# Kernel optimization log

Measured on AMD Instinct MI355X. Metric: run time of the kernel, lower is better.

## Reference

```python
import jax, jax.numpy as jnp
import numpy as np

N_USERS = 50000
N_ENTITIES = 100000
CHANNEL = 64
N_FACTORS = 4
N_REL = 9  # n_relations; weight has N_REL-1 rows
N_EDGES = 1_500_000
NNZ = 800_000
N_HOPS = 2


def _l2_normalize(x, eps=1e-12):
    # matches torch F.normalize(dim=1)
    n = jnp.sqrt(jnp.sum(x * x, axis=1, keepdims=True))
    return x / jnp.maximum(n, eps)


def _distance_correlation(t1, t2):
    # t1, t2: [d] rows of disen_weight_att (d = n_relations-1)
    ch = t1.shape[0]
    t1 = t1[:, None]
    t2 = t2[:, None]
    a_ = (t1 @ t1.T) * 2.0
    b_ = (t2 @ t2.T) * 2.0
    t1s = t1 ** 2
    t2s = t2 ** 2
    a = jnp.sqrt(jnp.maximum(t1s - a_ + t1s.T, 0.0) + 1e-8)
    b = jnp.sqrt(jnp.maximum(t2s - b_ + t2s.T, 0.0) + 1e-8)
    A = a - a.mean(axis=0, keepdims=True) - a.mean(axis=1, keepdims=True) + a.mean()
    B = b - b.mean(axis=0, keepdims=True) - b.mean(axis=1, keepdims=True) + b.mean()
    dcov_AB = jnp.sqrt(jnp.maximum((A * B).sum() / ch ** 2, 0.0) + 1e-8)
    dcov_AA = jnp.sqrt(jnp.maximum((A * A).sum() / ch ** 2, 0.0) + 1e-8)
    dcov_BB = jnp.sqrt(jnp.maximum((B * B).sum() / ch ** 2, 0.0) + 1e-8)
    return dcov_AB / jnp.sqrt(dcov_AA * dcov_BB + 1e-8)


def _cul_cor(disen_weight_att):
    cor = jnp.asarray(0.0, disen_weight_att.dtype)
    for i in range(N_FACTORS):
        for j in range(i + 1, N_FACTORS):
            cor = cor + _distance_correlation(disen_weight_att[i], disen_weight_att[j])
    return cor


def setup_inputs() -> dict:
    key = jax.random.key(0)
    ks = jax.random.split(key, 11)
    return {
        "user_emb": jax.random.normal(ks[0], (N_USERS, CHANNEL), jnp.float32) * 0.1,
        "entity_emb": jax.random.normal(ks[1], (N_ENTITIES, CHANNEL), jnp.float32) * 0.1,
        "latent_emb": jax.random.normal(ks[2], (N_FACTORS, CHANNEL), jnp.float32) * 0.1,
        "weight": jax.random.normal(ks[3], (N_REL - 1, CHANNEL), jnp.float32) * 0.1,
        "disen_weight_att": jax.random.normal(ks[4], (N_FACTORS, N_REL - 1), jnp.float32) * 0.1,
        "interact_vals": jax.random.uniform(ks[5], (NNZ,), jnp.float32),
        "head": jax.random.randint(ks[6], (N_EDGES,), 0, N_ENTITIES),
        "tail": jax.random.randint(ks[7], (N_EDGES,), 0, N_ENTITIES),
        "edge_type": jax.random.randint(ks[8], (N_EDGES,), 1, N_REL),  # in [1, N_REL-1]
        "interact_rows": jax.random.randint(ks[9], (NNZ,), 0, N_USERS),
        "interact_cols": jax.random.randint(ks[10], (NNZ,), 0, N_ENTITIES),
    }


def reference(user_emb, entity_emb, latent_emb, weight, disen_weight_att,
              interact_vals, head, tail, edge_type, interact_rows, interact_cols):
    n_entities = entity_emb.shape[0]
    n_users = user_emb.shape[0]
    cor = _cul_cor(disen_weight_att)

    entity_res = entity_emb
    user_res = user_emb
    ones_e = jnp.ones((head.shape[0],), entity_emb.dtype)
    cnt = jax.ops.segment_sum(ones_e, head, num_segments=n_entities)  # reused: head fixed
    cnt = jnp.maximum(cnt, 1.0)[:, None]

    for _ in range(N_HOPS):
        # KG aggregate: gather tail emb * relation emb, scatter-mean by head
        rel_emb = weight[edge_type - 1]                      # [E, C]
        msg = entity_emb[tail] * rel_emb                     # [E, C]
        entity_agg = jax.ops.segment_sum(msg, head, num_segments=n_entities) / cnt

        # user -> latent factor attention
        score = jax.nn.softmax(user_emb @ latent_emb.T, axis=1)   # [U, F]

        # user aggregate: sparse.mm(interact_mat, entity_emb)
        gathered = interact_vals[:, None] * entity_emb[interact_cols]  # [nnz, C]
        user_agg = jax.ops.segment_sum(gathered, interact_rows, num_segments=n_users)

        disen_weight = jax.nn.softmax(disen_weight_att, axis=-1) @ weight  # [F, C]
        mix = score @ disen_weight                                          # [U, C]
        user_new = user_agg * mix + user_agg

        entity_emb = _l2_normalize(entity_agg)
        user_emb = _l2_normalize(user_new)
        entity_res = entity_res + entity_emb
        user_res = user_res + user_emb

    return entity_res, user_res, cor
```

## Files before the change

kernel.cpp:

```cpp
#include <hip/hip_runtime.h>
#include <math.h>

constexpr int CH         = 64;
constexpr int N_USERS    = 50000;
constexpr int N_ENTITIES = 100000;
constexpr int N_FACTORS  = 4;
constexpr int N_RELM1    = 8;
constexpr int N_EDGES    = 1500000;
constexpr int NNZ        = 800000;

constexpr int NBE        = (N_ENTITIES + 255) / 256;
constexpr int NBU        = (N_USERS + 255) / 256;
constexpr int NBKT       = NBE + NBU;
constexpr int TOTAL      = N_EDGES + NNZ;
constexpr int IPB        = 8192;
constexpr int NBLK       = (TOTAL + IPB - 1) / IPB;
constexpr int ENT_BLOCKS = N_ENTITIES / 4;
constexpr int USR_BLOCKS = N_USERS / 4;

typedef unsigned int u32;

__device__ __forceinline__ u32 pack_bf16x2(float a, float b) {
    u32 ua = __float_as_uint(a), ub = __float_as_uint(b);
    u32 ra = (ua + 0x7FFFu + ((ua >> 16) & 1u)) >> 16;
    u32 rb = (ub + 0x7FFFu + ((ub >> 16) & 1u)) >> 16;
    return ra | (rb << 16);
}
__device__ __forceinline__ float bf_lo(u32 v) { return __uint_as_float(v << 16); }
__device__ __forceinline__ float bf_hi(u32 v) { return __uint_as_float(v & 0xFFFF0000u); }

__device__ __forceinline__ int coarse_bucket(int i, const int* __restrict__ head,
                                             const int* __restrict__ irows) {
    return (i < N_EDGES) ? (head[i] >> 8) : (NBE + (irows[i - N_EDGES] >> 8));
}

__global__ __launch_bounds__(256)
void count_coarse(const int* __restrict__ head, const int* __restrict__ irows,
                  int* __restrict__ H) {
    __shared__ int hist[NBKT];
    for (int j = threadIdx.x; j < NBKT; j += 256) hist[j] = 0;
    __syncthreads();
    int start = blockIdx.x * IPB;
    int end   = min(start + IPB, TOTAL);
    for (int i = start + threadIdx.x; i < end; i += 256)
        atomicAdd(&hist[coarse_bucket(i, head, irows)], 1);
    __syncthreads();
    for (int j = threadIdx.x; j < NBKT; j += 256)
        H[j * NBLK + blockIdx.x] = hist[j];
}

__global__ __launch_bounds__(64)
void scan_hcols(int* __restrict__ H, int* __restrict__ T) {
    int b = blockIdx.x, lane = threadIdx.x;
    int carry = 0;
    #pragma unroll
    for (int c = 0; c < (NBLK + 63) / 64; ++c) {
        int idx = c * 64 + lane;
        int v = (idx < NBLK) ? H[b * NBLK + idx] : 0;
        int incl = v;
        #pragma unroll
        for (int d = 1; d < 64; d <<= 1) {
            int u = __shfl_up(incl, d, 64);
            if (lane >= d) incl += u;
        }
        if (idx < NBLK) H[b * NBLK + idx] = carry + incl - v;
        carry += __shfl(incl, 63, 64);
    }
    if (lane == 0) T[b] = carry;
}

__global__ __launch_bounds__(1024)
void scan_buckets(const int* __restrict__ T, int* __restrict__ Bb) {
    __shared__ int lds[1024];
    int t = threadIdx.x;
    int v = (t < NBKT) ? T[t] : 0;
    lds[t] = v;
    __syncthreads();
    for (int d = 1; d < 1024; d <<= 1) {
        int u = (t >= d) ? lds[t - d] : 0;
        __syncthreads();
        lds[t] += u;
        __syncthreads();
    }
    if (t < NBKT) Bb[t] = lds[t] - v;
    if (t == NBKT - 1) Bb[NBKT] = lds[t];
}

__global__ __launch_bounds__(256)
void scatter_stage(const int* __restrict__ head, const int* __restrict__ tail,
                   const int* __restrict__ etype,
                   const int* __restrict__ irows, const int* __restrict__ icols,
                   const float* __restrict__ ivals,
                   const int* __restrict__ H, const int* __restrict__ Bb,
                   int2* __restrict__ stageE, int2* __restrict__ stageU,
                   float* __restrict__ stageUv) {
    __shared__ int cur[NBKT];
    for (int j = threadIdx.x; j < NBKT; j += 256)
        cur[j] = Bb[j] + H[j * NBLK + blockIdx.x];
    __syncthreads();
    int start = blockIdx.x * IPB;
    int end   = min(start + IPB, TOTAL);
    for (int i = start + threadIdx.x; i < end; i += 256) {
        if (i < N_EDGES) {
            int k   = head[i];
            int pay = tail[i] | ((etype[i] - 1) << 20);
            int pos = atomicAdd(&cur[k >> 8], 1);
            stageE[pos] = make_int2(k, pay);
        } else {
            int ii  = i - N_EDGES;
            int k   = irows[ii];
            int pos = atomicAdd(&cur[NBE + (k >> 8)], 1) - N_EDGES;
            stageU[pos]  = make_int2(k, icols[ii]);
            stageUv[pos] = ivals[ii];
        }
    }
}

__global__ __launch_bounds__(256)
void bin_fill(const int* __restrict__ Bb,
              const int2* __restrict__ stageE, const int2* __restrict__ stageU,
              const float* __restrict__ stageUv,
              int* __restrict__ offE, int* __restrict__ offU,
              int* __restrict__ elst, int* __restrict__ ucol,
              float* __restrict__ uval) {
    __shared__ int khist[256];
    __shared__ int cur[256];
    int b = blockIdx.x, t = threadIdx.x;
    khist[t] = 0;
    __syncthreads();
    if (b < NBE) {
        int lo = Bb[b], hi = Bb[b + 1];
        for (int i = lo + t; i < hi; i += 256)
            atomicAdd(&khist[stageE[i].x & 255], 1);
        __syncthreads();
        int v = khist[t];
        for (int d = 1; d < 256; d <<= 1) {
            int u = (t >= d) ? khist[t - d] : 0;
            __syncthreads();
            khist[t] += u;
            __syncthreads();
        }
        int excl = lo + khist[t] - v;
        int key  = b * 256 + t;
        if (key < N_ENTITIES) offE[key] = excl;
        cur[t] = excl;
        __syncthreads();
        for (int i = lo + t; i < hi; i += 256) {
            int2 s = stageE[i];
            int p = atomicAdd(&cur[s.x & 255], 1);
            elst[p] = s.y;
        }
        if (b == 0 && t == 0) offE[N_ENTITIES] = N_EDGES;
    } else {
        int lo = Bb[b] - N_EDGES, hi = Bb[b + 1] - N_EDGES;
        for (int i = lo + t; i < hi; i += 256)
            atomicAdd(&khist[stageU[i].x & 255], 1);
        __syncthreads();
        int v = khist[t];
        for (int d = 1; d < 256; d <<= 1) {
            int u = (t >= d) ? khist[t - d] : 0;
            __syncthreads();
            khist[t] += u;
            __syncthreads();
        }
        int excl = lo + khist[t] - v;
        int key  = (b - NBE) * 256 + t;
        if (key < N_USERS) offU[key] = excl;
        cur[t] = excl;
        __syncthreads();
        for (int i = lo + t; i < hi; i += 256) {
            int2 s = stageU[i];
            float vv = stageUv[i];
            int p = atomicAdd(&cur[s.x & 255], 1);
            ucol[p] = s.y;
            uval[p] = vv;
        }
        if (b == NBE && t == 0) offU[N_USERS] = NNZ;
    }
}

__global__ __launch_bounds__(256)
void to_bf16(const float* __restrict__ src, u32* __restrict__ dst, int n2) {
    int i = blockIdx.x * 256 + threadIdx.x;
    if (i < n2) {
        float2 f = ((const float2*)src)[i];
        dst[i] = pack_bf16x2(f.x, f.y);
    }
}

template <bool HOP0>
__global__ __launch_bounds__(256)
void hop_pass(const u32* __restrict__ entB,
              const float* __restrict__ usr_in,
              const float* __restrict__ weight, const float* __restrict__ latent,
              const float* __restrict__ dw,
              const int* __restrict__ offE, const int* __restrict__ elst,
              const int* __restrict__ offU, const int* __restrict__ ucol,
              const float* __restrict__ uval,
              u32* __restrict__ AeB_out,
              float* __restrict__ Au_out,
              float* __restrict__ ent_res, float* __restrict__ usr_res,
              const float* __restrict__ ent_base, const float* __restrict__ usr_base) {
    __shared__ float2 w_lds[N_RELM1 * 32];
    int lane = threadIdx.x & 63;
    int half = lane >> 5;
    int c2   = lane & 31;
    if (blockIdx.x < ENT_BLOCKS) {
        if (threadIdx.x < N_RELM1 * 32)
            w_lds[threadIdx.x] = ((const float2*)weight)[threadIdx.x];
        __syncthreads();
        int row = blockIdx.x * 4 + (threadIdx.x >> 6);
        int lo = offE[row], hi = offE[row + 1];
        float a0 = 0.0f, a1 = 0.0f;
        for (int k0 = lo; k0 < hi; k0 += 64) {
            int m = min(64, hi - k0);
            int p = (lane < m) ? elst[k0 + lane] : 0;
            int k = 0;
            for (; k + 3 < m; k += 4) {
                int pA = __shfl(p, k + half,     64);
                int pB = __shfl(p, k + 2 + half, 64);
                u32 xA = entB[(pA & 0xFFFFF) * 32 + c2];
                u32 xB = entB[(pB & 0xFFFFF) * 32 + c2];
                float2 wA = w_lds[(pA >> 20) * 32 + c2];
                float2 wB = w_lds[(pB >> 20) * 32 + c2];
                a0 += bf_lo(xA) * wA.x; a1 += bf_hi(xA) * wA.y;
                a0 += bf_lo(xB) * wB.x; a1 += bf_hi(xB) * wB.y;
            }
            for (; k < m; k += 2) {
                int kk = min(k + half, m - 1);
                float flag = (k + half < m) ? 1.0f : 0.0f;
                int pA = __shfl(p, kk, 64);
                u32 xA = entB[(pA & 0xFFFFF) * 32 + c2];
                float2 wA = w_lds[(pA >> 20) * 32 + c2];
                a0 += flag * bf_lo(xA) * wA.x;
                a1 += flag * bf_hi(xA) * wA.y;
            }
        }
        a0 += __shfl_xor(a0, 32, 64);
        a1 += __shfl_xor(a1, 32, 64);
        float s = a0 * a0 + a1 * a1;
        #pragma unroll
        for (int o = 1; o < 32; o <<= 1) s += __shfl_xor(s, o, 64);
        float inv = 1.0f / fmaxf(sqrtf(s), 1e-12f);
        float y0 = a0 * inv, y1 = a1 * inv;
        if (half == 0) {
            int idx = row * 32 + c2;
            if (HOP0) {
                AeB_out[idx] = pack_bf16x2(y0, y1);
                float2 base = ((const float2*)ent_base)[idx];
                ((float2*)ent_res)[idx] = make_float2(base.x + y0, base.y + y1);
            } else {
                float2 r = ((float2*)ent_res)[idx];
                ((float2*)ent_res)[idx] = make_float2(r.x + y0, r.y + y1);
            }
        }
    } else {
        int row = (blockIdx.x - ENT_BLOCKS) * 4 + (threadIdx.x >> 6);
        int idx = row * 32 + c2;
        float2 u  = ((const float2*)usr_in)[idx];
        float2 l0 = ((const float2*)latent)[0 * 32 + c2];
        float2 l1 = ((const float2*)latent)[1 * 32 + c2];
        float2 l2 = ((const float2*)latent)[2 * 32 + c2];
        float2 l3 = ((const float2*)latent)[3 * 32 + c2];
        float d0 = u.x * l0.x + u.y * l0.y;
        float d1 = u.x * l1.x + u.y * l1.y;
        float d2 = u.x * l2.x + u.y * l2.y;
        float d3 = u.x * l3.x + u.y * l3.y;
        #pragma unroll
        for (int o = 1; o < 32; o <<= 1) {
            d0 += __shfl_xor(d0, o, 64); d1 += __shfl_xor(d1, o, 64);
            d2 += __shfl_xor(d2, o, 64); d3 += __shfl_xor(d3, o, 64);
        }
        float mx = fmaxf(fmaxf(d0, d1), fmaxf(d2, d3));
        float e0 = expf(d0 - mx), e1 = expf(d1 - mx), e2 = expf(d2 - mx), e3 = expf(d3 - mx);
        float sinv = 1.0f / (e0 + e1 + e2 + e3);
        float2 w0 = ((const float2*)dw)[0 * 32 + c2];
        float2 w1 = ((const float2*)dw)[1 * 32 + c2];
        float2 w2 = ((const float2*)dw)[2 * 32 + c2];
        float2 w3 = ((const float2*)dw)[3 * 32 + c2];
        float mix0 = (e0 * w0.x + e1 * w1.x + e2 * w2.x + e3 * w3.x) * sinv;
        float mix1 = (e0 * w0.y + e1 * w1.y + e2 * w2.y + e3 * w3.y) * sinv;
        float a0 = 0.0f, a1 = 0.0f;
        int lo = offU[row], hi = offU[row + 1];
        for (int k0 = lo; k0 < hi; k0 += 64) {
            int m = min(64, hi - k0);
            int   cl = (lane < m) ? ucol[k0 + lane] : 0;
            float vv = (lane < m) ? uval[k0 + lane] : 0.0f;
            int k = 0;
            for (; k + 3 < m; k += 4) {
                int   cA = __shfl(cl, k + half,     64);
                int   cB = __shfl(cl, k + 2 + half, 64);
                float vA = __shfl(vv, k + half,     64);
                float vB = __shfl(vv, k + 2 + half, 64);
                u32 xA = entB[cA * 32 + c2];
                u32 xB = entB[cB * 32 + c2];
                a0 += vA * bf_lo(xA); a1 += vA * bf_hi(xA);
                a0 += vB * bf_lo(xB); a1 += vB * bf_hi(xB);
            }
            for (; k < m; k += 2) {
                int kk = min(k + half, m - 1);
                float flag = (k + half < m) ? 1.0f : 0.0f;
                int   cA = __shfl(cl, kk, 64);
                float vA = __shfl(vv, kk, 64) * flag;
                u32 xA = entB[cA * 32 + c2];
                a0 += vA * bf_lo(xA); a1 += vA * bf_hi(xA);
            }
        }
        a0 += __shfl_xor(a0, 32, 64);
        a1 += __shfl_xor(a1, 32, 64);
        float un0 = a0 * (1.0f + mix0);
        float un1 = a1 * (1.0f + mix1);
        float s = un0 * un0 + un1 * un1;
        #pragma unroll
        for (int o = 1; o < 32; o <<= 1) s += __shfl_xor(s, o, 64);
        float inv = 1.0f / fmaxf(sqrtf(s), 1e-12f);
        float y0 = un0 * inv, y1 = un1 * inv;
        if (half == 0) {
            if (HOP0) {
                ((float2*)Au_out)[idx] = make_float2(y0, y1);
                float2 base = ((const float2*)usr_base)[idx];
                ((float2*)usr_res)[idx] = make_float2(base.x + y0, base.y + y1);
            } else {
                float2 r = ((float2*)usr_res)[idx];
                ((float2*)usr_res)[idx] = make_float2(r.x + y0, r.y + y1);
            }
        }
    }
}

__global__ __launch_bounds__(384)
void discor_kernel(const float* __restrict__ att,
                   const float* __restrict__ weight,
                   float* __restrict__ dw,
                   float* __restrict__ cor_out) {
    __shared__ float part[6];
    if (blockIdx.x == 0) {
        if (threadIdx.x < 256) {
            int f = threadIdx.x >> 6;
            int c = threadIdx.x & 63;
            float m = -1e30f;
            #pragma unroll
            for (int j = 0; j < N_RELM1; ++j) m = fmaxf(m, att[f * N_RELM1 + j]);
            float s = 0.0f, w[N_RELM1];
            #pragma unroll
            for (int j = 0; j < N_RELM1; ++j) { w[j] = expf(att[f * N_RELM1 + j] - m); s += w[j]; }
            float acc = 0.0f;
            #pragma unroll
            for (int j = 0; j < N_RELM1; ++j) acc += w[j] * weight[j * CH + c];
            dw[f * CH + c] = acc / s;
        }
    } else {
        int w    = threadIdx.x >> 6;
        int lane = threadIdx.x & 63;
        const int pi[6] = {0, 0, 0, 1, 1, 2};
        const int pj[6] = {1, 2, 3, 2, 3, 3};
        int r = lane >> 3, c = lane & 7;
        const float* t1 = att + pi[w] * N_RELM1;
        const float* t2 = att + pj[w] * N_RELM1;
        float a  = sqrtf(fmaxf(t1[r] * t1[r] - 2.0f * t1[r] * t1[c] + t1[c] * t1[c], 0.0f) + 1e-8f);
        float bb = sqrtf(fmaxf(t2[r] * t2[r] - 2.0f * t2[r] * t2[c] + t2[c] * t2[c], 0.0f) + 1e-8f);
        float rsA = a, rsB = bb;
        #pragma unroll
        for (int o = 1; o < 8; o <<= 1) { rsA += __shfl_xor(rsA, o, 64); rsB += __shfl_xor(rsB, o, 64); }
        float csA = a, csB = bb;
        #pragma unroll
        for (int o = 8; o < 64; o <<= 1) { csA += __shfl_xor(csA, o, 64); csB += __shfl_xor(csB, o, 64); }
        float totA = rsA, totB = rsB;
        #pragma unroll
        for (int o = 8; o < 64; o <<= 1) { totA += __shfl_xor(totA, o, 64); totB += __shfl_xor(totB, o, 64); }
        float A = a  - csA * 0.125f - rsA * 0.125f + totA * (1.0f / 64.0f);
        float B = bb - csB * 0.125f - rsB * 0.125f + totB * (1.0f / 64.0f);
        float sAB = A * B, sAA = A * A, sBB = B * B;
        #pragma unroll
        for (int o = 1; o < 64; o <<= 1) {
            sAB += __shfl_xor(sAB, o, 64);
            sAA += __shfl_xor(sAA, o, 64);
            sBB += __shfl_xor(sBB, o, 64);
        }
        if (lane == 0) {
            float dAB = sqrtf(fmaxf(sAB * (1.0f / 64.0f), 0.0f) + 1e-8f);
            float dAA = sqrtf(fmaxf(sAA * (1.0f / 64.0f), 0.0f) + 1e-8f);
            float dBB = sqrtf(fmaxf(sBB * (1.0f / 64.0f), 0.0f) + 1e-8f);
            part[w] = dAB / sqrtf(dAA * dBB + 1e-8f);
        }
        __syncthreads();
        if (threadIdx.x == 0) {
            float s = 0.0f;
            for (int q = 0; q < 6; ++q) s += part[q];
            cor_out[0] = s;
        }
    }
}

extern "C" void kernel_launch(void* const* d_in, const int* in_sizes, int n_in,
                              void* d_out, int out_size, void* d_ws, size_t ws_size,
                              hipStream_t stream) {
    const float* user_emb   = (const float*)d_in[0];
    const float* entity_emb = (const float*)d_in[1];
    const float* latent     = (const float*)d_in[2];
    const float* weight     = (const float*)d_in[3];
    const float* att        = (const float*)d_in[4];
    const float* ivals      = (const float*)d_in[5];
    const int*   head       = (const int*)d_in[6];
    const int*   tail       = (const int*)d_in[7];
    const int*   etype      = (const int*)d_in[8];
    const int*   irows      = (const int*)d_in[9];
    const int*   icols      = (const int*)d_in[10];

    float* out     = (float*)d_out;
    float* ent_res = out;
    float* usr_res = out + (size_t)N_ENTITIES * CH;
    float* cor_out = out + (size_t)N_ENTITIES * CH + (size_t)N_USERS * CH;

    const size_t ENT_ELEMS = (size_t)N_ENTITIES * CH;
    const size_t USR_ELEMS = (size_t)N_USERS * CH;
    const int    ENT_PAIRS = (int)(ENT_ELEMS / 2);

    float* ws   = (float*)d_ws;
    u32*   entB = (u32*)ws;
    u32*   AeB  = entB + ENT_PAIRS;
    float* Au   = (float*)(AeB + ENT_PAIRS);
    float* dw   = Au + USR_ELEMS;
    int*   offE = (int*)(dw + N_FACTORS * CH);
    int*   offU = offE + N_ENTITIES + 1;
    int*   elst = offU + N_USERS + 1;
    int*   ucol = elst + N_EDGES;
    float* uval = (float*)(ucol + NNZ);
    int*   H    = (int*)(uval + NNZ);
    int*   T    = H + NBKT * NBLK;
    int*   Bb   = T + NBKT;
    int2*  stageE  = (int2*)entB;
    int2*  stageU  = ((int2*)entB) + N_EDGES;
    float* stageUv = (float*)(stageU + NNZ);

    discor_kernel<<<2, 384, 0, stream>>>(att, weight, dw, cor_out);

    count_coarse<<<NBLK, 256, 0, stream>>>(head, irows, H);
    scan_hcols<<<NBKT, 64, 0, stream>>>(H, T);
    scan_buckets<<<1, 1024, 0, stream>>>(T, Bb);
    scatter_stage<<<NBLK, 256, 0, stream>>>(head, tail, etype, irows, icols, ivals,
                                            H, Bb, stageE, stageU, stageUv);
    bin_fill<<<NBKT, 256, 0, stream>>>(Bb, stageE, stageU, stageUv,
                                       offE, offU, elst, ucol, uval);

    to_bf16<<<(ENT_PAIRS + 255) / 256, 256, 0, stream>>>(entity_emb, entB, ENT_PAIRS);

    hop_pass<true><<<ENT_BLOCKS + USR_BLOCKS, 256, 0, stream>>>(
        entB, user_emb, weight, latent, dw,
        offE, elst, offU, ucol, uval,
        AeB, Au, ent_res, usr_res, entity_emb, user_emb);

    hop_pass<false><<<ENT_BLOCKS + USR_BLOCKS, 256, 0, stream>>>(
        AeB, Au, weight, latent, dw,
        offE, elst, offU, ucol, uval,
        nullptr, nullptr, ent_res, usr_res, nullptr, nullptr);
}
```

Baseline: 400.0 us.

## Pack staging keys into 32-bit words, fuse bf16 conversion, widen gather loads

The sort staging buffers now pack the low 8 bits of the row key into spare bits of the payload, which halves the staging traffic in scatter_stage and bin_fill. Staging moves into the AeB region so the entity bf16 conversion can run early, fused into the discor kernel launch, removing one launch. The hop kernels now gather 16 bytes per lane, so one wave processes 8 edges at once with 8 lanes per row instead of 2 edges with 32 lanes. This cuts gather instruction count but raises register use and needs a longer cross-lane reduction.

```diff
diff --git a/kernel.cpp b/kernel.cpp
--- a/kernel.cpp
+++ b/kernel.cpp
@@ -92,7 +92,7 @@
                    const int* __restrict__ irows, const int* __restrict__ icols,
                    const float* __restrict__ ivals,
                    const int* __restrict__ H, const int* __restrict__ Bb,
-                   int2* __restrict__ stageE, int2* __restrict__ stageU,
+                   u32* __restrict__ stageE, u32* __restrict__ stageUc,
                    float* __restrict__ stageUv) {
     __shared__ int cur[NBKT];
     for (int j = threadIdx.x; j < NBKT; j += 256)
@@ -102,15 +102,15 @@
     int end   = min(start + IPB, TOTAL);
     for (int i = start + threadIdx.x; i < end; i += 256) {
         if (i < N_EDGES) {
-            int k   = head[i];
-            int pay = tail[i] | ((etype[i] - 1) << 20);
+            int k = head[i];
+            u32 pay = (u32)tail[i] | ((u32)(etype[i] - 1) << 20) | ((u32)(k & 255) << 24);
             int pos = atomicAdd(&cur[k >> 8], 1);
-            stageE[pos] = make_int2(k, pay);
+            stageE[pos] = pay;
         } else {
-            int ii  = i - N_EDGES;
-            int k   = irows[ii];
+            int ii = i - N_EDGES;
+            int k  = irows[ii];
             int pos = atomicAdd(&cur[NBE + (k >> 8)], 1) - N_EDGES;
-            stageU[pos]  = make_int2(k, icols[ii]);
+            stageUc[pos] = (u32)icols[ii] | ((u32)(k & 255) << 17);
             stageUv[pos] = ivals[ii];
         }
     }
@@ -118,7 +118,7 @@
 
 __global__ __launch_bounds__(256)
 void bin_fill(const int* __restrict__ Bb,
-              const int2* __restrict__ stageE, const int2* __restrict__ stageU,
+              const u32* __restrict__ stageE, const u32* __restrict__ stageUc,
               const float* __restrict__ stageUv,
               int* __restrict__ offE, int* __restrict__ offU,
               int* __restrict__ elst, int* __restrict__ ucol,
@@ -131,7 +131,7 @@
     if (b < NBE) {
         int lo = Bb[b], hi = Bb[b + 1];
         for (int i = lo + t; i < hi; i += 256)
-            atomicAdd(&khist[stageE[i].x & 255], 1);
+            atomicAdd(&khist[(stageE[i] >> 24) & 255], 1);
         __syncthreads();
         int v = khist[t];
         for (int d = 1; d < 256; d <<= 1) {
@@ -146,15 +146,15 @@
         cur[t] = excl;
         __syncthreads();
         for (int i = lo + t; i < hi; i += 256) {
-            int2 s = stageE[i];
-            int p = atomicAdd(&cur[s.x & 255], 1);
-            elst[p] = s.y;
+            u32 s = stageE[i];
+            int p = atomicAdd(&cur[(s >> 24) & 255], 1);
+            elst[p] = (int)(s & 0x00FFFFFFu);
         }
         if (b == 0 && t == 0) offE[N_ENTITIES] = N_EDGES;
     } else {
         int lo = Bb[b] - N_EDGES, hi = Bb[b + 1] - N_EDGES;
         for (int i = lo + t; i < hi; i += 256)
-            atomicAdd(&khist[stageU[i].x & 255], 1);
+            atomicAdd(&khist[(stageUc[i] >> 17) & 255], 1);
         __syncthreads();
         int v = khist[t];
         for (int d = 1; d < 256; d <<= 1) {
@@ -169,170 +169,31 @@
         cur[t] = excl;
         __syncthreads();
         for (int i = lo + t; i < hi; i += 256) {
-            int2 s = stageU[i];
+            u32 s = stageUc[i];
             float vv = stageUv[i];
-            int p = atomicAdd(&cur[s.x & 255], 1);
-            ucol[p] = s.y;
+            int p = atomicAdd(&cur[(s >> 17) & 255], 1);
+            ucol[p] = (int)(s & 0x1FFFFu);
             uval[p] = vv;
         }
         if (b == NBE && t == 0) offU[N_USERS] = NNZ;
     }
 }
 
-__global__ __launch_bounds__(256)
-void to_bf16(const float* __restrict__ src, u32* __restrict__ dst, int n2) {
-    int i = blockIdx.x * 256 + threadIdx.x;
-    if (i < n2) {
-        float2 f = ((const float2*)src)[i];
-        dst[i] = pack_bf16x2(f.x, f.y);
-    }
-}
-
-template <bool HOP0>
-__global__ __launch_bounds__(256)
-void hop_pass(const u32* __restrict__ entB,
-              const float* __restrict__ usr_in,
-              const float* __restrict__ weight, const float* __restrict__ latent,
-              const float* __restrict__ dw,
-              const int* __restrict__ offE, const int* __restrict__ elst,
-              const int* __restrict__ offU, const int* __restrict__ ucol,
-              const float* __restrict__ uval,
-              u32* __restrict__ AeB_out,
-              float* __restrict__ Au_out,
-              float* __restrict__ ent_res, float* __restrict__ usr_res,
-              const float* __restrict__ ent_base, const float* __restrict__ usr_base) {
-    __shared__ float2 w_lds[N_RELM1 * 32];
-    int lane = threadIdx.x & 63;
-    int half = lane >> 5;
-    int c2   = lane & 31;
-    if (blockIdx.x < ENT_BLOCKS) {
-        if (threadIdx.x < N_RELM1 * 32)
-            w_lds[threadIdx.x] = ((const float2*)weight)[threadIdx.x];
-        __syncthreads();
-        int row = blockIdx.x * 4 + (threadIdx.x >> 6);
-        int lo = offE[row], hi = offE[row + 1];
-        float a0 = 0.0f, a1 = 0.0f;
-        for (int k0 = lo; k0 < hi; k0 += 64) {
-            int m = min(64, hi - k0);
-            int p = (lane < m) ? elst[k0 + lane] : 0;
-            int k = 0;
-            for (; k + 3 < m; k += 4) {
-                int pA = __shfl(p, k + half,     64);
-                int pB = __shfl(p, k + 2 + half, 64);
-                u32 xA = entB[(pA & 0xFFFFF) * 32 + c2];
-                u32 xB = entB[(pB & 0xFFFFF) * 32 + c2];
-                float2 wA = w_lds[(pA >> 20) * 32 + c2];
-                float2 wB = w_lds[(pB >> 20) * 32 + c2];
-                a0 += bf_lo(xA) * wA.x; a1 += bf_hi(xA) * wA.y;
-                a0 += bf_lo(xB) * wB.x; a1 += bf_hi(xB) * wB.y;
-            }
-            for (; k < m; k += 2) {
-                int kk = min(k + half, m - 1);
-                float flag = (k + half < m) ? 1.0f : 0.0f;
-                int pA = __shfl(p, kk, 64);
-                u32 xA = entB[(pA & 0xFFFFF) * 32 + c2];
-                float2 wA = w_lds[(pA >> 20) * 32 + c2];
-                a0 += flag * bf_lo(xA) * wA.x;
-                a1 += flag * bf_hi(xA) * wA.y;
-            }
-        }
-        a0 += __shfl_xor(a0, 32, 64);
-        a1 += __shfl_xor(a1, 32, 64);
-        float s = a0 * a0 + a1 * a1;
-        #pragma unroll
-        for (int o = 1; o < 32; o <<= 1) s += __shfl_xor(s, o, 64);
-        float inv = 1.0f / fmaxf(sqrtf(s), 1e-12f);
-        float y0 = a0 * inv, y1 = a1 * inv;
-        if (half == 0) {
-            int idx = row * 32 + c2;
-            if (HOP0) {
-                AeB_out[idx] = pack_bf16x2(y0, y1);
-                float2 base = ((const float2*)ent_base)[idx];
-                ((float2*)ent_res)[idx] = make_float2(base.x + y0, base.y + y1);
-            } else {
-                float2 r = ((float2*)ent_res)[idx];
-                ((float2*)ent_res)[idx] = make_float2(r.x + y0, r.y + y1);
-            }
-        }
-    } else {
-        int row = (blockIdx.x - ENT_BLOCKS) * 4 + (threadIdx.x >> 6);
-        int idx = row * 32 + c2;
-        float2 u  = ((const float2*)usr_in)[idx];
-        float2 l0 = ((const float2*)latent)[0 * 32 + c2];
-        float2 l1 = ((const float2*)latent)[1 * 32 + c2];
-        float2 l2 = ((const float2*)latent)[2 * 32 + c2];
-        float2 l3 = ((const float2*)latent)[3 * 32 + c2];
-        float d0 = u.x * l0.x + u.y * l0.y;
-        float d1 = u.x * l1.x + u.y * l1.y;
-        float d2 = u.x * l2.x + u.y * l2.y;
-        float d3 = u.x * l3.x + u.y * l3.y;
-        #pragma unroll
-        for (int o = 1; o < 32; o <<= 1) {
-            d0 += __shfl_xor(d0, o, 64); d1 += __shfl_xor(d1, o, 64);
-            d2 += __shfl_xor(d2, o, 64); d3 += __shfl_xor(d3, o, 64);
-        }
-        float mx = fmaxf(fmaxf(d0, d1), fmaxf(d2, d3));
-        float e0 = expf(d0 - mx), e1 = expf(d1 - mx), e2 = expf(d2 - mx), e3 = expf(d3 - mx);
-        float sinv = 1.0f / (e0 + e1 + e2 + e3);
-        float2 w0 = ((const float2*)dw)[0 * 32 + c2];
-        float2 w1 = ((const float2*)dw)[1 * 32 + c2];
-        float2 w2 = ((const float2*)dw)[2 * 32 + c2];
-        float2 w3 = ((const float2*)dw)[3 * 32 + c2];
-        float mix0 = (e0 * w0.x + e1 * w1.x + e2 * w2.x + e3 * w3.x) * sinv;
-        float mix1 = (e0 * w0.y + e1 * w1.y + e2 * w2.y + e3 * w3.y) * sinv;
-        float a0 = 0.0f, a1 = 0.0f;
-        int lo = offU[row], hi = offU[row + 1];
-        for (int k0 = lo; k0 < hi; k0 += 64) {
-            int m = min(64, hi - k0);
-            int   cl = (lane < m) ? ucol[k0 + lane] : 0;
-            float vv = (lane < m) ? uval[k0 + lane] : 0.0f;
-            int k = 0;
-            for (; k + 3 < m; k += 4) {
-                int   cA = __shfl(cl, k + half,     64);
-                int   cB = __shfl(cl, k + 2 + half, 64);
-                float vA = __shfl(vv, k + half,     64);
-                float vB = __shfl(vv, k + 2 + half, 64);
-                u32 xA = entB[cA * 32 + c2];
-                u32 xB = entB[cB * 32 + c2];
-                a0 += vA * bf_lo(xA); a1 += vA * bf_hi(xA);
-                a0 += vB * bf_lo(xB); a1 += vB * bf_hi(xB);
-            }
-            for (; k < m; k += 2) {
-                int kk = min(k + half, m - 1);
-                float flag = (k + half < m) ? 1.0f : 0.0f;
-                int   cA = __shfl(cl, kk, 64);
-                float vA = __shfl(vv, kk, 64) * flag;
-                u32 xA = entB[cA * 32 + c2];
-                a0 += vA * bf_lo(xA); a1 += vA * bf_hi(xA);
-            }
-        }
-        a0 += __shfl_xor(a0, 32, 64);
-        a1 += __shfl_xor(a1, 32, 64);
-        float un0 = a0 * (1.0f + mix0);
-        float un1 = a1 * (1.0f + mix1);
-        float s = un0 * un0 + un1 * un1;
-        #pragma unroll
-        for (int o = 1; o < 32; o <<= 1) s += __shfl_xor(s, o, 64);
-        float inv = 1.0f / fmaxf(sqrtf(s), 1e-12f);
-        float y0 = un0 * inv, y1 = un1 * inv;
-        if (half == 0) {
-            if (HOP0) {
-                ((float2*)Au_out)[idx] = make_float2(y0, y1);
-                float2 base = ((const float2*)usr_base)[idx];
-                ((float2*)usr_res)[idx] = make_float2(base.x + y0, base.y + y1);
-            } else {
-                float2 r = ((float2*)usr_res)[idx];
-                ((float2*)usr_res)[idx] = make_float2(r.x + y0, r.y + y1);
-            }
-        }
-    }
-}
-
 __global__ __launch_bounds__(384)
-void discor_kernel(const float* __restrict__ att,
-                   const float* __restrict__ weight,
-                   float* __restrict__ dw,
-                   float* __restrict__ cor_out) {
+void discor_cvt(const float* __restrict__ att,
+                const float* __restrict__ weight,
+                const float* __restrict__ ent_src,
+                float* __restrict__ dw,
+                float* __restrict__ cor_out,
+                u32* __restrict__ entB, int n4) {
+    if (blockIdx.x >= 2) {
+        int i = (blockIdx.x - 2) * 384 + threadIdx.x;
+        if (i < n4) {
+            float4 f = ((const float4*)ent_src)[i];
+            ((uint2*)entB)[i] = make_uint2(pack_bf16x2(f.x, f.y), pack_bf16x2(f.z, f.w));
+        }
+        return;
+    }
     __shared__ float part[6];
     if (blockIdx.x == 0) {
         if (threadIdx.x < 256) {
@@ -392,6 +253,167 @@
     }
 }
 
+template <bool HOP0>
+__global__ __launch_bounds__(256)
+void hop_pass(const u32* __restrict__ entB,
+              const float* __restrict__ usr_in,
+              const float* __restrict__ weight, const float* __restrict__ latent,
+              const float* __restrict__ dw,
+              const int* __restrict__ offE, const int* __restrict__ elst,
+              const int* __restrict__ offU, const int* __restrict__ ucol,
+              const float* __restrict__ uval,
+              u32* __restrict__ AeB_out,
+              float* __restrict__ Au_out,
+              float* __restrict__ ent_res, float* __restrict__ usr_res,
+              const float* __restrict__ ent_base, const float* __restrict__ usr_base) {
+    __shared__ float4 w_lds[N_RELM1 * 16];
+    int lane = threadIdx.x & 63;
+    int oct  = lane >> 3;
+    int q    = lane & 7;
+    if (blockIdx.x < ENT_BLOCKS) {
+        if (threadIdx.x < N_RELM1 * 16)
+            w_lds[threadIdx.x] = ((const float4*)weight)[threadIdx.x];
+        __syncthreads();
+        int row = blockIdx.x * 4 + (threadIdx.x >> 6);
+        int lo = offE[row], hi = offE[row + 1];
+        float acc[8] = {0, 0, 0, 0, 0, 0, 0, 0};
+        for (int k0 = lo; k0 < hi; k0 += 64) {
+            int m = min(64, hi - k0);
+            int p = (lane < m) ? elst[k0 + lane] : 0;
+            for (int k = 0; k < m; k += 8) {
+                int  kk    = min(k + oct, m - 1);
+                bool valid = (k + oct) < m;
+                int pk = __shfl(p, kk, 64);
+                int tl = pk & 0xFFFFF;
+                int et = pk >> 20;
+                uint4 x = ((const uint4*)entB)[tl * 8 + q];
+                if (!valid) x = make_uint4(0u, 0u, 0u, 0u);
+                float4 wA = w_lds[et * 16 + q * 2];
+                float4 wB = w_lds[et * 16 + q * 2 + 1];
+                acc[0] += bf_lo(x.x) * wA.x; acc[1] += bf_hi(x.x) * wA.y;
+                acc[2] += bf_lo(x.y) * wA.z; acc[3] += bf_hi(x.y) * wA.w;
+                acc[4] += bf_lo(x.z) * wB.x; acc[5] += bf_hi(x.z) * wB.y;
+                acc[6] += bf_lo(x.w) * wB.z; acc[7] += bf_hi(x.w) * wB.w;
+            }
+        }
+        #pragma unroll
+        for (int i = 0; i < 8; ++i) {
+            acc[i] += __shfl_xor(acc[i], 8, 64);
+            acc[i] += __shfl_xor(acc[i], 16, 64);
+            acc[i] += __shfl_xor(acc[i], 32, 64);
+        }
+        float s = 0.0f;
+        #pragma unroll
+        for (int i = 0; i < 8; ++i) s += acc[i] * acc[i];
+        s += __shfl_xor(s, 1, 64); s += __shfl_xor(s, 2, 64); s += __shfl_xor(s, 4, 64);
+        float inv = 1.0f / fmaxf(sqrtf(s), 1e-12f);
+        if (oct == 0) {
+            float y[8];
+            #pragma unroll
+            for (int i = 0; i < 8; ++i) y[i] = acc[i] * inv;
+            int fidx = row * 16 + q * 2;
+            if (HOP0) {
+                ((uint4*)AeB_out)[row * 8 + q] = make_uint4(
+                    pack_bf16x2(y[0], y[1]), pack_bf16x2(y[2], y[3]),
+                    pack_bf16x2(y[4], y[5]), pack_bf16x2(y[6], y[7]));
+                float4 b0 = ((const float4*)ent_base)[fidx];
+                float4 b1 = ((const float4*)ent_base)[fidx + 1];
+                ((float4*)ent_res)[fidx]     = make_float4(b0.x + y[0], b0.y + y[1], b0.z + y[2], b0.w + y[3]);
+                ((float4*)ent_res)[fidx + 1] = make_float4(b1.x + y[4], b1.y + y[5], b1.z + y[6], b1.w + y[7]);
+            } else {
+                float4 r0 = ((const float4*)ent_res)[fidx];
+                float4 r1 = ((const float4*)ent_res)[fidx + 1];
+                ((float4*)ent_res)[fidx]     = make_float4(r0.x + y[0], r0.y + y[1], r0.z + y[2], r0.w + y[3]);
+                ((float4*)ent_res)[fidx + 1] = make_float4(r1.x + y[4], r1.y + y[5], r1.z + y[6], r1.w + y[7]);
+            }
+        }
+    } else {
+        int row = (blockIdx.x - ENT_BLOCKS) * 4 + (threadIdx.x >> 6);
+        int fidx = row * 16 + q * 2;
+        float4 u0 = ((const float4*)usr_in)[fidx];
+        float4 u1 = ((const float4*)usr_in)[fidx + 1];
+        float d[4];
+        #pragma unroll
+        for (int f = 0; f < 4; ++f) {
+            float4 l0 = ((const float4*)latent)[f * 16 + q * 2];
+            float4 l1 = ((const float4*)latent)[f * 16 + q * 2 + 1];
+            d[f] = u0.x * l0.x + u0.y * l0.y + u0.z * l0.z + u0.w * l0.w
+                 + u1.x * l1.x + u1.y * l1.y + u1.z * l1.z + u1.w * l1.w;
+            d[f] += __shfl_xor(d[f], 1, 64);
+            d[f] += __shfl_xor(d[f], 2, 64);
+            d[f] += __shfl_xor(d[f], 4, 64);
+        }
+        float mx = fmaxf(fmaxf(d[0], d[1]), fmaxf(d[2], d[3]));
+        float e0 = expf(d[0] - mx), e1 = expf(d[1] - mx);
+        float e2 = expf(d[2] - mx), e3 = expf(d[3] - mx);
+        float sinv = 1.0f / (e0 + e1 + e2 + e3);
+        float mix[8];
+        {
+            float4 w00 = ((const float4*)dw)[0 * 16 + q * 2], w01 = ((const float4*)dw)[0 * 16 + q * 2 + 1];
+            float4 w10 = ((const float4*)dw)[1 * 16 + q * 2], w11 = ((const float4*)dw)[1 * 16 + q * 2 + 1];
+            float4 w20 = ((const float4*)dw)[2 * 16 + q * 2], w21 = ((const float4*)dw)[2 * 16 + q * 2 + 1];
+            float4 w30 = ((const float4*)dw)[3 * 16 + q * 2], w31 = ((const float4*)dw)[3 * 16 + q * 2 + 1];
+            mix[0] = (e0 * w00.x + e1 * w10.x + e2 * w20.x + e3 * w30.x) * sinv;
+            mix[1] = (e0 * w00.y + e1 * w10.y + e2 * w20.y + e3 * w30.y) * sinv;
+            mix[2] = (e0 * w00.z + e1 * w10.z + e2 * w20.z + e3 * w30.z) * sinv;
+            mix[3] = (e0 * w00.w + e1 * w10.w + e2 * w20.w + e3 * w30.w) * sinv;
+            mix[4] = (e0 * w01.x + e1 * w11.x + e2 * w21.x + e3 * w31.x) * sinv;
+            mix[5] = (e0 * w01.y + e1 * w11.y + e2 * w21.y + e3 * w31.y) * sinv;
+            mix[6] = (e0 * w01.z + e1 * w11.z + e2 * w21.z + e3 * w31.z) * sinv;
+            mix[7] = (e0 * w01.w + e1 * w11.w + e2 * w21.w + e3 * w31.w) * sinv;
+        }
+        float acc[8] = {0, 0, 0, 0, 0, 0, 0, 0};
+        int lo = offU[row], hi = offU[row + 1];
+        for (int k0 = lo; k0 < hi; k0 += 64) {
+            int m = min(64, hi - k0);
+            int   cl = (lane < m) ? ucol[k0 + lane] : 0;
+            float vv = (lane < m) ? uval[k0 + lane] : 0.0f;
+            for (int k = 0; k < m; k += 8) {
+                int  kk    = min(k + oct, m - 1);
+                bool valid = (k + oct) < m;
+                int   ck = __shfl(cl, kk, 64);
+                float vk = __shfl(vv, kk, 64);
+                if (!valid) vk = 0.0f;
+                uint4 x = ((const uint4*)entB)[ck * 8 + q];
+                acc[0] += vk * bf_lo(x.x); acc[1] += vk * bf_hi(x.x);
+                acc[2] += vk * bf_lo(x.y); acc[3] += vk * bf_hi(x.y);
+                acc[4] += vk * bf_lo(x.z); acc[5] += vk * bf_hi(x.z);
+                acc[6] += vk * bf_lo(x.w); acc[7] += vk * bf_hi(x.w);
+            }
+        }
+        #pragma unroll
+        for (int i = 0; i < 8; ++i) {
+            acc[i] += __shfl_xor(acc[i], 8, 64);
+            acc[i] += __shfl_xor(acc[i], 16, 64);
+            acc[i] += __shfl_xor(acc[i], 32, 64);
+        }
+        float un[8];
+        float s = 0.0f;
+        #pragma unroll
+        for (int i = 0; i < 8; ++i) { un[i] = acc[i] * (1.0f + mix[i]); s += un[i] * un[i]; }
+        s += __shfl_xor(s, 1, 64); s += __shfl_xor(s, 2, 64); s += __shfl_xor(s, 4, 64);
+        float inv = 1.0f / fmaxf(sqrtf(s), 1e-12f);
+        if (oct == 0) {
+            float y[8];
+            #pragma unroll
+            for (int i = 0; i < 8; ++i) y[i] = un[i] * inv;
+            if (HOP0) {
+                ((float4*)Au_out)[fidx]     = make_float4(y[0], y[1], y[2], y[3]);
+                ((float4*)Au_out)[fidx + 1] = make_float4(y[4], y[5], y[6], y[7]);
+                float4 b0 = ((const float4*)usr_base)[fidx];
+                float4 b1 = ((const float4*)usr_base)[fidx + 1];
+                ((float4*)usr_res)[fidx]     = make_float4(b0.x + y[0], b0.y + y[1], b0.z + y[2], b0.w + y[3]);
+                ((float4*)usr_res)[fidx + 1] = make_float4(b1.x + y[4], b1.y + y[5], b1.z + y[6], b1.w + y[7]);
+            } else {
+                float4 r0 = ((const float4*)usr_res)[fidx];
+                float4 r1 = ((const float4*)usr_res)[fidx + 1];
+                ((float4*)usr_res)[fidx]     = make_float4(r0.x + y[0], r0.y + y[1], r0.z + y[2], r0.w + y[3]);
+                ((float4*)usr_res)[fidx + 1] = make_float4(r1.x + y[4], r1.y + y[5], r1.z + y[6], r1.w + y[7]);
+            }
+        }
+    }
+}
+
 extern "C" void kernel_launch(void* const* d_in, const int* in_sizes, int n_in,
                               void* d_out, int out_size, void* d_ws, size_t ws_size,
                               hipStream_t stream) {
@@ -415,6 +437,7 @@
     const size_t ENT_ELEMS = (size_t)N_ENTITIES * CH;
     const size_t USR_ELEMS = (size_t)N_USERS * CH;
     const int    ENT_PAIRS = (int)(ENT_ELEMS / 2);
+    const int    ENT_QUADS = (int)(ENT_ELEMS / 4);
 
     float* ws   = (float*)d_ws;
     u32*   entB = (u32*)ws;
@@ -429,21 +452,21 @@
     int*   H    = (int*)(uval + NNZ);
     int*   T    = H + NBKT * NBLK;
     int*   Bb   = T + NBKT;
-    int2*  stageE  = (int2*)entB;
-    int2*  stageU  = ((int2*)entB) + N_EDGES;
-    float* stageUv = (float*)(stageU + NNZ);
-
-    discor_kernel<<<2, 384, 0, stream>>>(att, weight, dw, cor_out);
+    u32*   stageE  = AeB;
+    u32*   stageUc = stageE + N_EDGES;
+    float* stageUv = (float*)(stageUc + NNZ);
+
+    const int cvtBlocks = (ENT_QUADS + 383) / 384;
+    discor_cvt<<<2 + cvtBlocks, 384, 0, stream>>>(att, weight, entity_emb,
+                                                  dw, cor_out, entB, ENT_QUADS);
 
     count_coarse<<<NBLK, 256, 0, stream>>>(head, irows, H);
     scan_hcols<<<NBKT, 64, 0, stream>>>(H, T);
     scan_buckets<<<1, 1024, 0, stream>>>(T, Bb);
     scatter_stage<<<NBLK, 256, 0, stream>>>(head, tail, etype, irows, icols, ivals,
-                                            H, Bb, stageE, stageU, stageUv);
-    bin_fill<<<NBKT, 256, 0, stream>>>(Bb, stageE, stageU, stageUv,
+                                            H, Bb, stageE, stageUc, stageUv);
+    bin_fill<<<NBKT, 256, 0, stream>>>(Bb, stageE, stageUc, stageUv,
                                        offE, offU, elst, ucol, uval);
-
-    to_bf16<<<(ENT_PAIRS + 255) / 256, 256, 0, stream>>>(entity_emb, entB, ENT_PAIRS);
 
     hop_pass<true><<<ENT_BLOCKS + USR_BLOCKS, 256, 0, stream>>>(
         entB, user_emb, weight, latent, dw,
```

After: 444.4 us. 11.1% more time.
